# Kernel tuning notes

Hardware: AMD Instinct MI355X
Metric: run time of the kernel (lower is better)

## Reference

```python
import jax, jax.numpy as jnp
import numpy as np


def setup_inputs() -> dict:
    key = jax.random.key(0)
    ks = jax.random.split(key, 8)
    B, C, W, H = 8, 128, 64, 64
    Cp = C // 8  # f/g projection channels (in_channels > 8)
    s = 0.05
    return {
        "x": jax.random.normal(ks[0], (B, C, W, H), jnp.float32),
        "Wf": jax.random.normal(ks[1], (Cp, C), jnp.float32) * s,
        "bf": jax.random.normal(ks[2], (Cp,), jnp.float32) * s,
        "Wg": jax.random.normal(ks[3], (Cp, C), jnp.float32) * s,
        "bg": jax.random.normal(ks[4], (Cp,), jnp.float32) * s,
        "Wh": jax.random.normal(ks[5], (C, C), jnp.float32) * s,
        "bh": jax.random.normal(ks[6], (C,), jnp.float32) * s,
        "gamma": jax.random.normal(ks[7], (1,), jnp.float32) * s,
    }


def reference(x, Wf, bf, Wg, bg, Wh, bh, gamma):
    B, C, W, H = x.shape
    N = W * H
    xf = x.reshape(B, C, N)  # flatten spatial
    # 1x1 convs == per-position channel matmuls
    f = jnp.einsum("oc,bcn->bon", Wf, xf) + bf[None, :, None]  # [B,C',N]
    g = jnp.einsum("oc,bcn->bon", Wg, xf) + bg[None, :, None]  # [B,C',N]
    h = jnp.einsum("oc,bcn->bon", Wh, xf) + bh[None, :, None]  # [B,C,N]
    # scores[b,n,m] = sum_c f[b,c,n] * g[b,c,m]  (no scaling, as in source)
    scores = jnp.einsum("bcn,bcm->bnm", f, g)  # [B,N,N]
    attn = jax.nn.softmax(scores, axis=-1)
    # attended[b,c,m] = sum_n h[b,c,n] * attn[b,n,m]  (h_x @ attention_map)
    attended = jnp.einsum("bcn,bnm->bcm", h, attn)  # [B,C,N]
    return x + gamma * attended.reshape(B, C, W, H)
```

## Files before the change

### kernel.cpp

```cpp
#include <hip/hip_runtime.h>
#include <hip/hip_bf16.h>

#define BB 8
#define CC 128
#define NN 4096
#define LOG2E 1.44269504088896340736f

typedef __attribute__((ext_vector_type(4))) float f32x4;
typedef __attribute__((ext_vector_type(4))) short s16x4;
typedef __attribute__((ext_vector_type(8))) short s16x8;

__device__ inline short f2bf(float f){
  unsigned u = __float_as_uint(f);
  u += 0x7FFFu + ((u >> 16) & 1u);
  return (short)(u >> 16);
}
__device__ inline unsigned pack2(float e0, float e1){
  return __builtin_amdgcn_perm(__float_as_uint(e1), __float_as_uint(e0), 0x07060302u);
}

__device__ inline s16x8 frag_read(const char* base, int row, int kk, int g){
  const int m = row & 31;
  const char* rp = base + row*256;
  s16x4 lo = *(const s16x4*)(rp + (((kk*8 + g)     ^ m) << 3));
  s16x4 hi = *(const s16x4*)(rp + (((kk*8 + 4 + g) ^ m) << 3));
  s16x8 r = {lo[0],lo[1],lo[2],lo[3],hi[0],hi[1],hi[2],hi[3]};
  return r;
}

__global__ __launch_bounds__(256) void k_proj(
    const float* __restrict__ x,  const float* __restrict__ Wf, const float* __restrict__ bf,
    const float* __restrict__ Wg, const float* __restrict__ bg,
    const float* __restrict__ Wh, const float* __restrict__ bh,
    short* __restrict__ fT, short* __restrict__ gT, short* __restrict__ hP)
{
  __shared__ __align__(16) char sx[16384];
  __shared__ __align__(16) char sw[40960];

  const int blk = blockIdx.x;
  const int b = blk & 7, ntile = blk >> 3;
  const int n0 = ntile * 64;
  const int tid = threadIdx.x;

  {
    const int cbase = tid >> 4;
    const int nj = (tid & 15) * 4;
    #pragma unroll
    for (int p = 0; p < 8; ++p){
      const int c = p*16 + cbase;
      f32x4 v = *(const f32x4*)(x + ((size_t)(b*128 + c))*NN + n0 + nj);
      #pragma unroll
      for (int e = 0; e < 4; ++e){
        const int n = nj + e;
        const int off = n*256 + ((((c>>2) ^ (n & 31))) << 3) + ((c & 3) << 1);
        *(short*)(sx + off) = f2bf(v[e]);
      }
    }
  }
  {
    #pragma unroll
    for (int p = 0; p < 20; ++p){
      const int id = p*256 + tid;
      const int row = id >> 5;
      const int q = id & 31;
      const float* src; float scale = 1.0f;
      if (row < 16)      { src = Wf + row*128;      scale = LOG2E; }
      else if (row < 32) { src = Wg + (row-16)*128; }
      else               { src = Wh + (row-32)*128; }
      f32x4 v = *(const f32x4*)(src + q*4);
      unsigned u0 = pack2(v[0]*scale, v[1]*scale);
      unsigned u1 = pack2(v[2]*scale, v[3]*scale);
      const int off = row*256 + ((q ^ (row & 31)) << 3);
      *(unsigned long long*)(sw + off) = ((unsigned long long)u1 << 32) | u0;
    }
  }
  __syncthreads();

  const int w = tid >> 6, l = tid & 63;
  const int g = l >> 4, lm = l & 15;
  const int nn = w*16 + lm;
  const int nglob = n0 + w*16 + lm;

  s16x8 xf[4];
  #pragma unroll
  for (int kk = 0; kk < 4; ++kk) xf[kk] = frag_read(sx, nn, kk, g);

  {
    f32x4 acc;
    f32x4 bv = *(const f32x4*)(bf + 4*g);
    #pragma unroll
    for (int i=0;i<4;++i) acc[i] = bv[i] * LOG2E;
    #pragma unroll
    for (int kk = 0; kk < 4; ++kk)
      acc = __builtin_amdgcn_mfma_f32_16x16x32_bf16(frag_read(sw, lm, kk, g), xf[kk], acc, 0,0,0);
    unsigned u0 = pack2(acc[0], acc[1]);
    unsigned u1 = pack2(acc[2], acc[3]);
    *(unsigned long long*)(fT + ((size_t)b*NN + nglob)*16 + 4*g) = ((unsigned long long)u1 << 32) | u0;
  }
  {
    f32x4 acc = *(const f32x4*)(bg + 4*g);
    #pragma unroll
    for (int kk = 0; kk < 4; ++kk)
      acc = __builtin_amdgcn_mfma_f32_16x16x32_bf16(frag_read(sw, 16+lm, kk, g), xf[kk], acc, 0,0,0);
    unsigned u0 = pack2(acc[0], acc[1]);
    unsigned u1 = pack2(acc[2], acc[3]);
    *(unsigned long long*)(gT + ((size_t)b*NN + nglob)*16 + 4*g) = ((unsigned long long)u1 << 32) | u0;
  }
  {
    const int nc  = ntile*2 + (w >> 1);
    const int tau = w & 1;
    #pragma unroll
    for (int ct = 0; ct < 8; ++ct){
      const float bb = bh[ct*16 + lm];
      f32x4 acc = {bb, bb, bb, bb};
      #pragma unroll
      for (int kk = 0; kk < 4; ++kk)
        acc = __builtin_amdgcn_mfma_f32_16x16x32_bf16(xf[kk], frag_read(sw, 32 + ct*16 + lm, kk, g), acc, 0,0,0);
      unsigned u0 = pack2(acc[0], acc[1]);
      unsigned u1 = pack2(acc[2], acc[3]);
      const int row = ct*64 + g*16 + lm;
      *(unsigned long long*)((char*)hP + (((size_t)(b*128 + nc))*512 + row)*16 + tau*8)
          = ((unsigned long long)u1 << 32) | u0;
    }
  }
}

__global__ __launch_bounds__(512,4) void k_stats(
    const short* __restrict__ fT, const short* __restrict__ gT, float* __restrict__ Lrow)
{
  __shared__ float sm[2][4][16];
  const int blk = blockIdx.x;
  const int b = blk & 7, ntile = blk >> 3;
  const int tid = threadIdx.x;
  const int w = tid >> 6, l = tid & 63;
  const int g = l >> 4, lm = l & 15;
  const int ns = w & 3, mh = w >> 2;
  const int n0 = ntile*64 + ns*16;
  const f32x4 zero4 = {0.f,0.f,0.f,0.f};

  s16x4 f4 = *(const s16x4*)(fT + ((size_t)b*NN + n0 + lm)*16 + 4*g);
  s16x8 fa = {f4[0],f4[1],f4[2],f4[3],0,0,0,0};

  const short* gTb = gT + ((size_t)b*NN + mh*2048 + lm)*16 + 4*g;

  f32x4 rs = {0.f,0.f,0.f,0.f};
  s16x4 gc[4], gn[4];
  #pragma unroll
  for (int j=0;j<4;++j) gc[j] = *(const s16x4*)(gTb + j*256);

  #pragma unroll 1
  for (int it=0; it<32; ++it){
    const int nx = (it < 31) ? it+1 : 31;
    #pragma unroll
    for (int j=0;j<4;++j) gn[j] = *(const s16x4*)(gTb + nx*1024 + j*256);
    #pragma unroll
    for (int j=0;j<4;++j){
      s16x8 gb = {gc[j][0],gc[j][1],gc[j][2],gc[j][3],0,0,0,0};
      f32x4 d = __builtin_amdgcn_mfma_f32_16x16x32_bf16(fa, gb, zero4, 0,0,0);
      #pragma unroll
      for (int i=0;i<4;++i) rs[i] += __builtin_amdgcn_exp2f(d[i]);
    }
    #pragma unroll
    for (int j=0;j<4;++j) gc[j] = gn[j];
  }
  #pragma unroll
  for (int i=0;i<4;++i){
    #pragma unroll
    for (int mask=1; mask<16; mask<<=1) rs[i] += __shfl_xor(rs[i], mask);
  }
  if (lm == 0){
    #pragma unroll
    for (int i=0;i<4;++i) sm[mh][ns][4*g+i] = rs[i];
  }
  __syncthreads();
  if (mh == 0 && lm == 0){
    #pragma unroll
    for (int i=0;i<4;++i){
      float z = rs[i] + sm[1][ns][4*g+i];
      Lrow[(size_t)b*NN + n0 + 4*g + i] = -__log2f(z);
    }
  }
}

__global__ __launch_bounds__(512,2) void k_attend(
    const float* __restrict__ x, const short* __restrict__ fT, const short* __restrict__ gT,
    const short* __restrict__ hP, const float* __restrict__ Lrow,
    const float* __restrict__ gamma, float* __restrict__ out)
{
  __shared__ __align__(16) char lds[32768];

  const int blk = blockIdx.x;
  const int b = blk & 7, mtile = blk >> 3;
  const int tid = threadIdx.x;
  const int w = tid >> 6, l = tid & 63;
  const int g = l >> 4, lm = l & 15;
  const int mw = w & 1, nq = w >> 1;
  const int m0w = mtile*128 + mw*64;
  const f32x4 zero4 = {0.f,0.f,0.f,0.f};

  const short* fTb = fT + ((size_t)b*NN + nq*1024 + lm)*16 + 4*g;
  const float* Lb  = Lrow + (size_t)b*NN + nq*1024 + 4*g;
  const char*  hB  = (const char*)hP + (((size_t)(b*128 + nq*32))*512 + l)*16;

  s16x8 gb[4];
  #pragma unroll
  for (int mt=0; mt<4; ++mt){
    s16x4 g4 = *(const s16x4*)(gT + ((size_t)b*NN + m0w + mt*16 + lm)*16 + 4*g);
    s16x8 t = {g4[0],g4[1],g4[2],g4[3],0,0,0,0};
    gb[mt] = t;
  }

  f32x4 acc[4][8];
  #pragma unroll
  for (int mt=0;mt<4;++mt)
    #pragma unroll
    for (int cs=0;cs<8;++cs) acc[mt][cs] = zero4;

  s16x4 fa_c0 = *(const s16x4*)(fTb);
  s16x4 fa_c1 = *(const s16x4*)(fTb + 256);
  f32x4 C0 = *(const f32x4*)(Lb);
  f32x4 C1 = *(const f32x4*)(Lb + 16);

  #pragma unroll 1
  for (int it=0; it<32; ++it){
    s16x8 hb[8];
    #pragma unroll
    for (int cs=0; cs<8; ++cs) hb[cs] = *(const s16x8*)(hB + it*8192 + cs*1024);

    s16x4 pfa0, pfa1; f32x4 pC0, pC1;
    if (it < 31){
      pfa0 = *(const s16x4*)(fTb + (it+1)*512);
      pfa1 = *(const s16x4*)(fTb + (it+1)*512 + 256);
      pC0  = *(const f32x4*)(Lb + (it+1)*32);
      pC1  = *(const f32x4*)(Lb + (it+1)*32 + 16);
    }

    s16x8 fa0 = {fa_c0[0],fa_c0[1],fa_c0[2],fa_c0[3],0,0,0,0};
    s16x8 fa1 = {fa_c1[0],fa_c1[1],fa_c1[2],fa_c1[3],0,0,0,0};

    __builtin_amdgcn_s_setprio(1);
    s16x8 A[4];
    #pragma unroll
    for (int mt=0; mt<4; ++mt){
      f32x4 d0 = __builtin_amdgcn_mfma_f32_16x16x32_bf16(fa0, gb[mt], C0, 0,0,0);
      f32x4 d1 = __builtin_amdgcn_mfma_f32_16x16x32_bf16(fa1, gb[mt], C1, 0,0,0);
      union { unsigned u[4]; s16x8 v; } P;
      P.u[0] = pack2(__builtin_amdgcn_exp2f(d0[0]), __builtin_amdgcn_exp2f(d0[1]));
      P.u[1] = pack2(__builtin_amdgcn_exp2f(d0[2]), __builtin_amdgcn_exp2f(d0[3]));
      P.u[2] = pack2(__builtin_amdgcn_exp2f(d1[0]), __builtin_amdgcn_exp2f(d1[1]));
      P.u[3] = pack2(__builtin_amdgcn_exp2f(d1[2]), __builtin_amdgcn_exp2f(d1[3]));
      A[mt] = P.v;
    }

    #pragma unroll
    for (int cs=0; cs<8; ++cs){
      #pragma unroll
      for (int mt=0; mt<4; ++mt)
        acc[mt][cs] = __builtin_amdgcn_mfma_f32_16x16x32_bf16(A[mt], hb[cs], acc[mt][cs], 0,0,0);
    }
    __builtin_amdgcn_s_setprio(0);

    fa_c0 = pfa0; fa_c1 = pfa1; C0 = pC0; C1 = pC1;
  }

  float* redA = (float*)lds;
  float* redB = (float*)(lds + 16384);
  const float gm = gamma[0];
  #pragma unroll
  for (int mt=0; mt<4; ++mt){
    if (nq == 1 || nq == 3){
      float* rp = (nq==1)? redA : redB;
      #pragma unroll
      for (int cs=0; cs<8; ++cs)
        *(f32x4*)(rp + (cs*128 + mw*64 + l)*4) = acc[mt][cs];
    }
    __syncthreads();
    if (nq == 0 || nq == 2){
      const float* rp = (nq==0)? redA : redB;
      #pragma unroll
      for (int cs=0; cs<8; ++cs)
        acc[mt][cs] += *(const f32x4*)(rp + (cs*128 + mw*64 + l)*4);
    }
    __syncthreads();
    if (nq == 2){
      #pragma unroll
      for (int cs=0; cs<8; ++cs)
        *(f32x4*)(redA + (cs*128 + mw*64 + l)*4) = acc[mt][cs];
    }
    __syncthreads();
    if (nq == 0){
      #pragma unroll
      for (int cs=0; cs<8; ++cs){
        f32x4 r = *(const f32x4*)(redA + (cs*128 + mw*64 + l)*4);
        f32x4 a = acc[mt][cs] + r;
        const int c = cs*16 + lm;
        const size_t base = ((size_t)(b*128 + c))*NN + m0w + mt*16 + 4*g;
        f32x4 xv = *(const f32x4*)(x + base);
        f32x4 ov;
        #pragma unroll
        for (int i=0;i<4;++i) ov[i] = xv[i] + gm*a[i];
        *(f32x4*)(out + base) = ov;
      }
    }
    __syncthreads();
  }
}

extern "C" void kernel_launch(void* const* d_in, const int* in_sizes, int n_in,
                              void* d_out, int out_size, void* d_ws, size_t ws_size,
                              hipStream_t stream)
{
  const float* x     = (const float*)d_in[0];
  const float* Wf    = (const float*)d_in[1];
  const float* bf    = (const float*)d_in[2];
  const float* Wg    = (const float*)d_in[3];
  const float* bg    = (const float*)d_in[4];
  const float* Wh    = (const float*)d_in[5];
  const float* bh    = (const float*)d_in[6];
  const float* gamma = (const float*)d_in[7];
  float* out = (float*)d_out;

  short* fT   = (short*)d_ws;
  short* gT   = fT + (size_t)BB*NN*16;
  short* hP   = gT + (size_t)BB*NN*16;
  float* Lrow = (float*)(hP + (size_t)BB*CC*NN);

  k_proj  <<<BB*64, 256, 0, stream>>>(x, Wf, bf, Wg, bg, Wh, bh, fT, gT, hP);
  k_stats <<<BB*64, 512, 0, stream>>>(fT, gT, Lrow);
  k_attend<<<BB*32, 512, 0, stream>>>(x, fT, gT, hP, Lrow, gamma, out);
}
```

Before: 70.17 us.

## Software-pipeline attention loop: compute next P tile and prefetch h ahead

Restructures the main attention loop into a software pipeline. The score MFMA plus exp2 for the next tile is computed while the current tile's P@h MFMAs run, and each h fragment is reloaded right after its last use so the next iteration's h is in flight during compute. f/L prefetch moves two iterations ahead. This hides global load latency and the exp dependency chain, at the cost of more live registers (A_cur/A_nxt, hb), which may lower occupancy or cause spills.

Result: no change. 70.44 us (+0.4%).

```diff
diff --git a/kernel.cpp b/kernel.cpp
--- a/kernel.cpp
+++ b/kernel.cpp
@@ -216,30 +216,19 @@
     #pragma unroll
     for (int cs=0;cs<8;++cs) acc[mt][cs] = zero4;
 
-  s16x4 fa_c0 = *(const s16x4*)(fTb);
-  s16x4 fa_c1 = *(const s16x4*)(fTb + 256);
+  s16x8 hb[8];
+  #pragma unroll
+  for (int cs=0; cs<8; ++cs) hb[cs] = *(const s16x8*)(hB + cs*1024);
+
+  s16x4 fa0v = *(const s16x4*)(fTb);
+  s16x4 fa1v = *(const s16x4*)(fTb + 256);
   f32x4 C0 = *(const f32x4*)(Lb);
   f32x4 C1 = *(const f32x4*)(Lb + 16);
 
-  #pragma unroll 1
-  for (int it=0; it<32; ++it){
-    s16x8 hb[8];
-    #pragma unroll
-    for (int cs=0; cs<8; ++cs) hb[cs] = *(const s16x8*)(hB + it*8192 + cs*1024);
-
-    s16x4 pfa0, pfa1; f32x4 pC0, pC1;
-    if (it < 31){
-      pfa0 = *(const s16x4*)(fTb + (it+1)*512);
-      pfa1 = *(const s16x4*)(fTb + (it+1)*512 + 256);
-      pC0  = *(const f32x4*)(Lb + (it+1)*32);
-      pC1  = *(const f32x4*)(Lb + (it+1)*32 + 16);
-    }
-
-    s16x8 fa0 = {fa_c0[0],fa_c0[1],fa_c0[2],fa_c0[3],0,0,0,0};
-    s16x8 fa1 = {fa_c1[0],fa_c1[1],fa_c1[2],fa_c1[3],0,0,0,0};
-
-    __builtin_amdgcn_s_setprio(1);
-    s16x8 A[4];
+  s16x8 A_cur[4], A_nxt[4];
+  {
+    s16x8 fa0 = {fa0v[0],fa0v[1],fa0v[2],fa0v[3],0,0,0,0};
+    s16x8 fa1 = {fa1v[0],fa1v[1],fa1v[2],fa1v[3],0,0,0,0};
     #pragma unroll
     for (int mt=0; mt<4; ++mt){
       f32x4 d0 = __builtin_amdgcn_mfma_f32_16x16x32_bf16(fa0, gb[mt], C0, 0,0,0);
@@ -249,18 +238,53 @@
       P.u[1] = pack2(__builtin_amdgcn_exp2f(d0[2]), __builtin_amdgcn_exp2f(d0[3]));
       P.u[2] = pack2(__builtin_amdgcn_exp2f(d1[0]), __builtin_amdgcn_exp2f(d1[1]));
       P.u[3] = pack2(__builtin_amdgcn_exp2f(d1[2]), __builtin_amdgcn_exp2f(d1[3]));
-      A[mt] = P.v;
+      A_cur[mt] = P.v;
+    }
+  }
+  fa0v = *(const s16x4*)(fTb + 512);
+  fa1v = *(const s16x4*)(fTb + 512 + 256);
+  C0   = *(const f32x4*)(Lb + 32);
+  C1   = *(const f32x4*)(Lb + 32 + 16);
+
+  #pragma unroll 1
+  for (int it=0; it<32; ++it){
+    const int nx  = (it < 31) ? it+1 : 31;
+    const int nx2 = (it < 30) ? it+2 : 31;
+
+    __builtin_amdgcn_s_setprio(1);
+    {
+      s16x8 fa0 = {fa0v[0],fa0v[1],fa0v[2],fa0v[3],0,0,0,0};
+      s16x8 fa1 = {fa1v[0],fa1v[1],fa1v[2],fa1v[3],0,0,0,0};
+      #pragma unroll
+      for (int mt=0; mt<4; ++mt){
+        f32x4 d0 = __builtin_amdgcn_mfma_f32_16x16x32_bf16(fa0, gb[mt], C0, 0,0,0);
+        f32x4 d1 = __builtin_amdgcn_mfma_f32_16x16x32_bf16(fa1, gb[mt], C1, 0,0,0);
+        union { unsigned u[4]; s16x8 v; } P;
+        P.u[0] = pack2(__builtin_amdgcn_exp2f(d0[0]), __builtin_amdgcn_exp2f(d0[1]));
+        P.u[1] = pack2(__builtin_amdgcn_exp2f(d0[2]), __builtin_amdgcn_exp2f(d0[3]));
+        P.u[2] = pack2(__builtin_amdgcn_exp2f(d1[0]), __builtin_amdgcn_exp2f(d1[1]));
+        P.u[3] = pack2(__builtin_amdgcn_exp2f(d1[2]), __builtin_amdgcn_exp2f(d1[3]));
+        A_nxt[mt] = P.v;
+      }
     }
 
     #pragma unroll
     for (int cs=0; cs<8; ++cs){
-      #pragma unroll
-      for (int mt=0; mt<4; ++mt)
-        acc[mt][cs] = __builtin_amdgcn_mfma_f32_16x16x32_bf16(A[mt], hb[cs], acc[mt][cs], 0,0,0);
+      acc[0][cs] = __builtin_amdgcn_mfma_f32_16x16x32_bf16(A_cur[0], hb[cs], acc[0][cs], 0,0,0);
+      acc[1][cs] = __builtin_amdgcn_mfma_f32_16x16x32_bf16(A_cur[1], hb[cs], acc[1][cs], 0,0,0);
+      acc[2][cs] = __builtin_amdgcn_mfma_f32_16x16x32_bf16(A_cur[2], hb[cs], acc[2][cs], 0,0,0);
+      acc[3][cs] = __builtin_amdgcn_mfma_f32_16x16x32_bf16(A_cur[3], hb[cs], acc[3][cs], 0,0,0);
+      hb[cs] = *(const s16x8*)(hB + nx*8192 + cs*1024);
     }
     __builtin_amdgcn_s_setprio(0);
 
-    fa_c0 = pfa0; fa_c1 = pfa1; C0 = pC0; C1 = pC1;
+    fa0v = *(const s16x4*)(fTb + nx2*512);
+    fa1v = *(const s16x4*)(fTb + nx2*512 + 256);
+    C0   = *(const f32x4*)(Lb + nx2*32);
+    C1   = *(const f32x4*)(Lb + nx2*32 + 16);
+
+    #pragma unroll
+    for (int mt=0; mt<4; ++mt) A_cur[mt] = A_nxt[mt];
   }
 
   float* redA = (float*)lds;
```

## Split attend blocks to 64 columns with 4 waves; pack x channel pairs

Applied to the files above, without the earlier changes.

k_attend now uses 256-thread blocks covering 64 output columns each, with twice as many blocks (512), so the grid fills more CUs on the device. The cost is that each block's h loads are shared by fewer waves, so global traffic for h roughly doubles. The prefetch of f and L is made unconditional by clamping the index, which removes a branch. k_proj now loads two channels at once and writes packed 32-bit bf16 pairs into LDS, halving the number of LDS stores.

New measurement: 69.17 us. No clear change (-1.4%).

```diff
diff --git a/kernel.cpp b/kernel.cpp
--- a/kernel.cpp
+++ b/kernel.cpp
@@ -43,17 +43,18 @@
   const int tid = threadIdx.x;
 
   {
-    const int cbase = tid >> 4;
+    const int cpair = tid >> 4;
     const int nj = (tid & 15) * 4;
     #pragma unroll
-    for (int p = 0; p < 8; ++p){
-      const int c = p*16 + cbase;
-      f32x4 v = *(const f32x4*)(x + ((size_t)(b*128 + c))*NN + n0 + nj);
+    for (int p = 0; p < 4; ++p){
+      const int c0 = p*32 + cpair*2;
+      f32x4 v0 = *(const f32x4*)(x + ((size_t)(b*128 + c0    ))*NN + n0 + nj);
+      f32x4 v1 = *(const f32x4*)(x + ((size_t)(b*128 + c0 + 1))*NN + n0 + nj);
       #pragma unroll
       for (int e = 0; e < 4; ++e){
         const int n = nj + e;
-        const int off = n*256 + ((((c>>2) ^ (n & 31))) << 3) + ((c & 3) << 1);
-        *(short*)(sx + off) = f2bf(v[e]);
+        const int off = n*256 + ((((c0>>2) ^ (n & 31))) << 3) + ((c0 & 3) << 1);
+        *(unsigned*)(sx + off) = pack2(v0[e], v1[e]);
       }
     }
   }
@@ -182,20 +183,19 @@
   }
 }
 
-__global__ __launch_bounds__(512,2) void k_attend(
+__global__ __launch_bounds__(256,2) void k_attend(
     const float* __restrict__ x, const short* __restrict__ fT, const short* __restrict__ gT,
     const short* __restrict__ hP, const float* __restrict__ Lrow,
     const float* __restrict__ gamma, float* __restrict__ out)
 {
-  __shared__ __align__(16) char lds[32768];
+  __shared__ __align__(16) char lds[16384];
 
   const int blk = blockIdx.x;
   const int b = blk & 7, mtile = blk >> 3;
   const int tid = threadIdx.x;
-  const int w = tid >> 6, l = tid & 63;
+  const int nq = tid >> 6, l = tid & 63;
   const int g = l >> 4, lm = l & 15;
-  const int mw = w & 1, nq = w >> 1;
-  const int m0w = mtile*128 + mw*64;
+  const int m0w = mtile*64;
   const f32x4 zero4 = {0.f,0.f,0.f,0.f};
 
   const short* fTb = fT + ((size_t)b*NN + nq*1024 + lm)*16 + 4*g;
@@ -223,17 +223,16 @@
 
   #pragma unroll 1
   for (int it=0; it<32; ++it){
+    const int nx = (it < 31) ? it+1 : 31;
+
     s16x8 hb[8];
     #pragma unroll
     for (int cs=0; cs<8; ++cs) hb[cs] = *(const s16x8*)(hB + it*8192 + cs*1024);
 
-    s16x4 pfa0, pfa1; f32x4 pC0, pC1;
-    if (it < 31){
-      pfa0 = *(const s16x4*)(fTb + (it+1)*512);
-      pfa1 = *(const s16x4*)(fTb + (it+1)*512 + 256);
-      pC0  = *(const f32x4*)(Lb + (it+1)*32);
-      pC1  = *(const f32x4*)(Lb + (it+1)*32 + 16);
-    }
+    s16x4 pfa0 = *(const s16x4*)(fTb + nx*512);
+    s16x4 pfa1 = *(const s16x4*)(fTb + nx*512 + 256);
+    f32x4 pC0  = *(const f32x4*)(Lb + nx*32);
+    f32x4 pC1  = *(const f32x4*)(Lb + nx*32 + 16);
 
     s16x8 fa0 = {fa_c0[0],fa_c0[1],fa_c0[2],fa_c0[3],0,0,0,0};
     s16x8 fa1 = {fa_c1[0],fa_c1[1],fa_c1[2],fa_c1[3],0,0,0,0};
@@ -264,7 +263,7 @@
   }
 
   float* redA = (float*)lds;
-  float* redB = (float*)(lds + 16384);
+  float* redB = (float*)(lds + 8192);
   const float gm = gamma[0];
   #pragma unroll
   for (int mt=0; mt<4; ++mt){
@@ -272,26 +271,26 @@
       float* rp = (nq==1)? redA : redB;
       #pragma unroll
       for (int cs=0; cs<8; ++cs)
-        *(f32x4*)(rp + (cs*128 + mw*64 + l)*4) = acc[mt][cs];
+        *(f32x4*)(rp + (cs*64 + l)*4) = acc[mt][cs];
     }
     __syncthreads();
     if (nq == 0 || nq == 2){
       const float* rp = (nq==0)? redA : redB;
       #pragma unroll
       for (int cs=0; cs<8; ++cs)
-        acc[mt][cs] += *(const f32x4*)(rp + (cs*128 + mw*64 + l)*4);
+        acc[mt][cs] += *(const f32x4*)(rp + (cs*64 + l)*4);
     }
     __syncthreads();
     if (nq == 2){
       #pragma unroll
       for (int cs=0; cs<8; ++cs)
-        *(f32x4*)(redA + (cs*128 + mw*64 + l)*4) = acc[mt][cs];
+        *(f32x4*)(redA + (cs*64 + l)*4) = acc[mt][cs];
     }
     __syncthreads();
     if (nq == 0){
       #pragma unroll
       for (int cs=0; cs<8; ++cs){
-        f32x4 r = *(const f32x4*)(redA + (cs*128 + mw*64 + l)*4);
+        f32x4 r = *(const f32x4*)(redA + (cs*64 + l)*4);
         f32x4 a = acc[mt][cs] + r;
         const int c = cs*16 + lm;
         const size_t base = ((size_t)(b*128 + c))*NN + m0w + mt*16 + 4*g;
@@ -327,5 +326,5 @@
 
   k_proj  <<<BB*64, 256, 0, stream>>>(x, Wf, bf, Wg, bg, Wh, bh, fT, gT, hP);
   k_stats <<<BB*64, 512, 0, stream>>>(fT, gT, Lrow);
-  k_attend<<<BB*32, 512, 0, stream>>>(x, fT, gT, hP, Lrow, gamma, out);
-}
+  k_attend<<<BB*64, 256, 0, stream>>>(x, fT, gT, hP, Lrow, gamma, out);
+}
```
